# Kernel tuning notes

Hardware: AMD Instinct MI355X
Metric: run time of the kernel (lower is better)

Reference implementation:

```python
import jax, jax.numpy as jnp
import numpy as np

B, S, D, H = 2, 2048, 1024, 16
DK = D // H


def setup_inputs() -> dict:
    key = jax.random.key(0)
    ks = jax.random.split(key, 8)
    q = jax.random.normal(ks[0], (B, S, D), dtype=jnp.float32)
    k = jax.random.normal(ks[1], (B, S, D), dtype=jnp.float32)
    v = jax.random.normal(ks[2], (B, S, D), dtype=jnp.float32)
    mask = jax.random.randint(ks[3], (B, 1, S, S), 0, 2, dtype=jnp.int32)
    sc = 1.0 / np.sqrt(D)
    Wq = jax.random.normal(ks[4], (D, D), dtype=jnp.float32) * sc
    Wk = jax.random.normal(ks[5], (D, D), dtype=jnp.float32) * sc
    Wv = jax.random.normal(ks[6], (D, D), dtype=jnp.float32) * sc
    Wo = jax.random.normal(ks[7], (D, D), dtype=jnp.float32) * sc
    return {"q": q, "k": k, "v": v, "mask": mask, "Wq": Wq, "Wk": Wk, "Wv": Wv, "Wo": Wo}


def reference(q, k, v, mask, Wq, Wk, Wv, Wo):
    # Linear projections (torch Linear: x @ W.T; bias=False). Weights here stored
    # as [D, D] applied as x @ W (equivalent parameterization).
    query = q @ Wq  # [B,S,D]
    key = k @ Wk
    value = v @ Wv
    # split heads -> [B,H,S,DK]
    query = query.reshape(B, S, H, DK).transpose(0, 2, 1, 3)
    key = key.reshape(B, S, H, DK).transpose(0, 2, 1, 3)
    value = value.reshape(B, S, H, DK).transpose(0, 2, 1, 3)
    scores = jnp.einsum('bhqd,bhkd->bhqk', query, key) / jnp.sqrt(jnp.float32(DK))
    scores = jnp.where(mask == 0, jnp.float32(-1e9), scores)
    probs = jax.nn.softmax(scores, axis=-1)  # dropout p=0.0 -> identity
    x = jnp.einsum('bhqk,bhkd->bhqd', probs, value)
    x = x.transpose(0, 2, 1, 3).reshape(B, S, D)
    return x @ Wo
```

## Files before the change

### kernel.cpp

```cpp
#include <hip/hip_runtime.h>
#include <hip/hip_bf16.h>
#include <math.h>

#define B_ 2
#define S_ 2048
#define D_ 1024
#define H_ 16
#define DK_ 64
#define SW_ (S_ / 64)

typedef unsigned short u16;
typedef unsigned int u32;
typedef unsigned long long u64;
typedef __attribute__((ext_vector_type(8))) short short8;
typedef __attribute__((ext_vector_type(4))) float float4_;
typedef __attribute__((ext_vector_type(4))) unsigned int uint4_;

static __device__ inline u16 f_to_bf16(float f) {
    union { float f; u32 i; } x; x.f = f;
    u32 r = x.i + 0x7fff + ((x.i >> 16) & 1);
    return (u16)(r >> 16);
}

static __device__ __forceinline__ u32 cvtpk(float a, float b) {
    u32 r;
    asm("v_cvt_pk_bf16_f32 %0, %1, %2" : "=v"(r) : "v"(a), "v"(b));
    return r;
}

static __device__ __forceinline__ float fast_exp2(float x) {
#if __has_builtin(__builtin_amdgcn_exp2f)
    return __builtin_amdgcn_exp2f(x);
#else
    return exp2f(x);
#endif
}

static __device__ inline void gl_lds16(const u16* g, u16* l) {
    __builtin_amdgcn_global_load_lds((const __attribute__((address_space(1))) void*)g,
                                     (__attribute__((address_space(3))) void*)l, 16, 0, 0);
}

__global__ __launch_bounds__(256) void prep(const float* __restrict__ q,
                                            const float* __restrict__ k,
                                            const float* __restrict__ v,
                                            const int* __restrict__ mask,
                                            const float* __restrict__ W0,
                                            const float* __restrict__ W1,
                                            const float* __restrict__ W2,
                                            const float* __restrict__ W3,
                                            u16* __restrict__ qb, u16* __restrict__ kb,
                                            u16* __restrict__ vb,
                                            u16* __restrict__ T0, u16* __restrict__ T1,
                                            u16* __restrict__ T2, u16* __restrict__ T3,
                                            u64* __restrict__ mpk) {
    __shared__ float tile[32][33];
    int gx = blockIdx.x, tid = threadIdx.x;
    if (gx < 6144) {
        int z = gx >> 11;
        int bx = gx & 2047;
        const float* s = (z == 0) ? q : ((z == 1) ? k : v);
        u16* d = (z == 0) ? qb : ((z == 1) ? kb : vb);
        int i = (bx * 256 + tid) * 8;
        #pragma unroll
        for (int j = 0; j < 8; ++j) d[i + j] = f_to_bf16(s[i + j]);
    } else if (gx < 10240) {
        int g2 = gx - 6144;
        int z = g2 >> 10;
        int rem = g2 & 1023;
        const float* W = (z == 0) ? W0 : ((z == 1) ? W1 : ((z == 2) ? W2 : W3));
        u16* Wt = (z == 0) ? T0 : ((z == 1) ? T1 : ((z == 2) ? T2 : T3));
        int k0 = (rem >> 5) * 32, n0 = (rem & 31) * 32;
        int tx = tid & 31, ty = tid >> 5;
        #pragma unroll
        for (int i2 = 0; i2 < 4; ++i2) {
            int row = ty + i2 * 8;
            tile[row][tx] = W[(size_t)(k0 + row) * D_ + n0 + tx];
        }
        __syncthreads();
        #pragma unroll
        for (int i2 = 0; i2 < 4; ++i2) {
            int row = ty + i2 * 8;
            Wt[(size_t)(n0 + row) * D_ + k0 + tx] = f_to_bf16(tile[tx][row]);
        }
    } else {
        int g3 = gx - 10240;
        int wv = (g3 * 256 + tid) >> 6;
        int lane = tid & 63;
        #pragma unroll
        for (int i2 = 0; i2 < 8; ++i2) {
            int wd = wv * 8 + i2;
            u64 bits = __ballot(mask[(size_t)wd * 64 + lane] != 0);
            if (lane == 0) mpk[wd] = bits;
        }
    }
}

static __device__ __forceinline__ void gemm128_body(u16* lds,
                                                    const u16* __restrict__ A,
                                                    const u16* __restrict__ Bt,
                                                    int K, float4_ (&acc)[4][4]) {
    u16* ldsA = lds;
    u16* ldsB = lds + 4096;
    int tm = blockIdx.x, tn = blockIdx.y;
    int t = threadIdx.x, l = t & 63;
    int w = t >> 6, wr = w >> 1, wc = w & 1;
    int colL = l & 15, grp = l >> 4;
    int sw4 = (grp ^ ((colL >> 1) & 3)) << 3;
    int f0 = t, f1 = t + 256;
    int row0 = f0 >> 2, kc0 = (((f0 & 3) ^ ((f0 >> 3) & 3)) << 3);
    int row1 = f1 >> 2, kc1 = (((f1 & 3) ^ ((f1 >> 3) & 3)) << 3);
    const u16* gA0 = A  + (size_t)(tm * 128 + row0) * K + kc0;
    const u16* gA1 = A  + (size_t)(tm * 128 + row1) * K + kc1;
    const u16* gB0 = Bt + (size_t)(tn * 128 + row0) * K + kc0;
    const u16* gB1 = Bt + (size_t)(tn * 128 + row1) * K + kc1;

    #pragma unroll
    for (int mi = 0; mi < 4; ++mi)
        #pragma unroll
        for (int ni = 0; ni < 4; ++ni)
            acc[mi][ni] = (float4_){0.f, 0.f, 0.f, 0.f};

    for (int k0 = 0; k0 < K; k0 += 32) {
        __syncthreads();
        gl_lds16(gA0 + k0, ldsA + f0 * 8);
        gl_lds16(gA1 + k0, ldsA + f1 * 8);
        gl_lds16(gB0 + k0, ldsB + f0 * 8);
        gl_lds16(gB1 + k0, ldsB + f1 * 8);
        __syncthreads();
        short8 a[4], b[4];
        #pragma unroll
        for (int mi = 0; mi < 4; ++mi)
            a[mi] = *(const short8*)&ldsA[(wr * 64 + mi * 16 + colL) * 32 + sw4];
        #pragma unroll
        for (int ni = 0; ni < 4; ++ni)
            b[ni] = *(const short8*)&ldsB[(wc * 64 + ni * 16 + colL) * 32 + sw4];
        #pragma unroll
        for (int mi = 0; mi < 4; ++mi)
            #pragma unroll
            for (int ni = 0; ni < 4; ++ni)
                acc[mi][ni] = __builtin_amdgcn_mfma_f32_16x16x32_bf16(a[mi], b[ni], acc[mi][ni], 0, 0, 0);
    }
}

__global__ __launch_bounds__(256, 3) void gemm_qkv(const u16* __restrict__ qb,
                                                   const u16* __restrict__ kb,
                                                   const u16* __restrict__ vb,
                                                   const u16* __restrict__ Wqt,
                                                   const u16* __restrict__ Wkt,
                                                   const u16* __restrict__ Wvt,
                                                   u16* __restrict__ Qp,
                                                   u16* __restrict__ Kp,
                                                   u16* __restrict__ Vt) {
    __shared__ u16 lds[8192];
    int z = blockIdx.z;
    const u16* A  = (z == 0) ? qb  : ((z == 1) ? kb  : vb);
    const u16* Bt = (z == 0) ? Wqt : ((z == 1) ? Wkt : Wvt);
    float4_ acc[4][4];
    gemm128_body(lds, A, Bt, D_, acc);

    int tm = blockIdx.x, tn = blockIdx.y;
    int t = threadIdx.x, l = t & 63;
    int w = t >> 6, wr = w >> 1, wc = w & 1;
    int colL = l & 15, grp = l >> 4;

    if (z < 2) {
        u16* Y = (z == 0) ? Qp : Kp;
        float sc = (z == 0) ? (0.125f * 1.44269504f) : 1.0f;
        #pragma unroll
        for (int mi = 0; mi < 4; ++mi)
            #pragma unroll
            for (int ni = 0; ni < 4; ++ni)
                #pragma unroll
                for (int r = 0; r < 4; ++r)
                    Y[(size_t)(tm * 128 + wr * 64 + mi * 16 + grp * 4 + r) * D_
                      + tn * 128 + wc * 64 + ni * 16 + colL] = f_to_bf16(acc[mi][ni][r] * sc);
    } else {
        int tok_base = tm * 128 + wr * 64;
        int bb = tok_base >> 11;
        int s_hi = tok_base & (S_ - 1);
        #pragma unroll
        for (int mi = 0; mi < 4; ++mi)
            #pragma unroll
            for (int ni = 0; ni < 4; ++ni) {
                int n  = tn * 128 + wc * 64 + ni * 16 + colL;
                int hh = n >> 6, dk = n & 63;
                u16* vp = Vt + ((size_t)(bb * H_ + hh) * DK_ + dk) * S_ + s_hi;
                #pragma unroll
                for (int r = 0; r < 4; ++r) {
                    int m = mi * 16 + grp * 4 + r;
                    int mp_ = ((m >> 5) & 1) * 32 + ((m >> 2) & 3) * 8 + ((m >> 4) & 1) * 4 + (m & 3);
                    vp[mp_] = f_to_bf16(acc[mi][ni][r]);
                }
            }
    }
}

__global__ __launch_bounds__(256, 3) void gemm_out(const u16* __restrict__ Xa,
                                                   const u16* __restrict__ Wot,
                                                   float* __restrict__ out) {
    __shared__ u16 lds[8192];
    float4_ acc[4][4];
    gemm128_body(lds, Xa, Wot, D_, acc);

    int tm = blockIdx.x, tn = blockIdx.y;
    int t = threadIdx.x, l = t & 63;
    int w = t >> 6, wr = w >> 1, wc = w & 1;
    int colL = l & 15, grp = l >> 4;
    #pragma unroll
    for (int mi = 0; mi < 4; ++mi)
        #pragma unroll
        for (int ni = 0; ni < 4; ++ni)
            #pragma unroll
            for (int r = 0; r < 4; ++r)
                out[(size_t)(tm * 128 + wr * 64 + mi * 16 + grp * 4 + r) * D_
                    + tn * 128 + wc * 64 + ni * 16 + colL] = acc[mi][ni][r];
}

__global__ __launch_bounds__(256, 2) void attn128(const u16* __restrict__ Qp,
                                                  const u16* __restrict__ Kp,
                                                  const u16* __restrict__ Vt,
                                                  const u64* __restrict__ mp,
                                                  u16* __restrict__ Xa) {
    __shared__ u16 ldsK[2 * 128 * 64];
    __shared__ u16 ldsV[2 * 2 * 64 * 64];

    int bid = blockIdx.x;
    int qt = bid & 15, h = (bid >> 4) & 15, b = bid >> 8;
    int t = threadIdx.x, l = t & 63, w = t >> 6;
    int colL = l & 15, grp = l >> 4;

    const u16* qbA = Qp + (size_t)(b * S_ + qt * 128 + w * 32 + colL) * D_ + h * DK_;
    const u16* qbB = qbA + (size_t)16 * D_;
    short8 qfA0 = *(const short8*)(qbA + grp * 8);
    short8 qfA1 = *(const short8*)(qbA + 32 + grp * 8);
    short8 qfB0 = *(const short8*)(qbB + grp * 8);
    short8 qfB1 = *(const short8*)(qbB + 32 + grp * 8);

    const u16* gK[4];
    const u16* gV[4];
    int fofs[4];
    #pragma unroll
    for (int i = 0; i < 4; ++i) {
        int f = t + 256 * i;
        fofs[i] = f * 8;
        int krow = f >> 3, kch = (((f & 7) ^ (krow & 7)) << 3);
        gK[i] = Kp + (size_t)(b * S_ + krow) * D_ + h * DK_ + kch;
        int hreg = f >> 9, fp = f & 511;
        int vrow = fp >> 3, vch = (((fp & 7) ^ (vrow & 7)) << 3);
        gV[i] = Vt + ((size_t)(b * H_ + h) * DK_ + vrow) * S_ + hreg * 64 + vch;
    }

    int sw8 = (grp ^ (colL & 7)) << 3;

    short8 onesb;
    #pragma unroll
    for (int j = 0; j < 8; ++j) onesb[j] = (short)0x3F80;

    float4_ laccA = (float4_){0.f, 0.f, 0.f, 0.f};
    float4_ laccB = (float4_){0.f, 0.f, 0.f, 0.f};
    float4_ oA[4], oB[4];
    #pragma unroll
    for (int nt = 0; nt < 4; ++nt) {
        oA[nt] = (float4_){0.f, 0.f, 0.f, 0.f};
        oB[nt] = (float4_){0.f, 0.f, 0.f, 0.f};
    }

    const u64* mrA = mp + (size_t)(b * S_ + qt * 128 + w * 32 + colL) * SW_;
    const u64* mrB = mrA + (size_t)16 * SW_;

    #pragma unroll
    for (int i = 0; i < 4; ++i) {
        gl_lds16(gK[i], ldsK + fofs[i]);
        gl_lds16(gV[i], ldsV + fofs[i]);
    }
    __syncthreads();

    int cur = 0;
    for (int kt = 0; kt < S_; kt += 128) {
        u64 mwA0 = mrA[(kt >> 6)];
        u64 mwA1 = mrA[(kt >> 6) + 1];
        u64 mwB0 = mrB[(kt >> 6)];
        u64 mwB1 = mrB[(kt >> 6) + 1];

        if (kt + 128 < S_) {
            int nb = (cur ^ 1) * 8192;
            #pragma unroll
            for (int i = 0; i < 4; ++i) {
                gl_lds16(gK[i] + (size_t)(kt + 128) * D_, ldsK + nb + fofs[i]);
                gl_lds16(gV[i] + (kt + 128),              ldsV + nb + fofs[i]);
            }
        }

        const u16* K_ = ldsK + cur * 8192;
        const u16* V_ = ldsV + cur * 8192;

        float4_ sA[8], sB[8];
        __builtin_amdgcn_s_setprio(1);
        #pragma unroll
        for (int nt = 0; nt < 8; ++nt) {
            int ro = (nt * 16 + colL) * 64;
            short8 kf0 = *(const short8*)&K_[ro + sw8];
            short8 kf1 = *(const short8*)&K_[ro + (sw8 ^ 32)];
            sA[nt] = (float4_){0.f, 0.f, 0.f, 0.f};
            sA[nt] = __builtin_amdgcn_mfma_f32_16x16x32_bf16(kf0, qfA0, sA[nt], 0, 0, 0);
            sA[nt] = __builtin_amdgcn_mfma_f32_16x16x32_bf16(kf1, qfA1, sA[nt], 0, 0, 0);
            sB[nt] = (float4_){0.f, 0.f, 0.f, 0.f};
            sB[nt] = __builtin_amdgcn_mfma_f32_16x16x32_bf16(kf0, qfB0, sB[nt], 0, 0, 0);
            sB[nt] = __builtin_amdgcn_mfma_f32_16x16x32_bf16(kf1, qfB1, sB[nt], 0, 0, 0);
        }
        __builtin_amdgcn_s_setprio(0);

        u64 mshA0 = mwA0 >> (grp * 4), mshA1 = mwA1 >> (grp * 4);
        u64 mshB0 = mwB0 >> (grp * 4), mshB1 = mwB1 >> (grp * 4);
        #pragma unroll
        for (int nt = 0; nt < 8; ++nt) {
            u32 bitsA = ((u32)((nt < 4 ? mshA0 : mshA1) >> ((nt & 3) * 16))) & 15u;
            u32 bitsB = ((u32)((nt < 4 ? mshB0 : mshB1) >> ((nt & 3) * 16))) & 15u;
            #pragma unroll
            for (int r = 0; r < 4; ++r) {
                float pA = fast_exp2(sA[nt][r]);
                float pB = fast_exp2(sB[nt][r]);
                u32 keepA = 0u - ((bitsA >> r) & 1u);
                u32 keepB = 0u - ((bitsB >> r) & 1u);
                union { float f; u32 i; } ua, ub;
                ua.f = pA; ua.i &= keepA; sA[nt][r] = ua.f;
                ub.f = pB; ub.i &= keepB; sB[nt][r] = ub.f;
            }
        }

        short8 pfA[4], pfB[4];
        #pragma unroll
        for (int j = 0; j < 4; ++j) {
            uint4_ Ax = { cvtpk(sA[2 * j][0], sA[2 * j][1]), cvtpk(sA[2 * j][2], sA[2 * j][3]),
                          cvtpk(sA[2 * j + 1][0], sA[2 * j + 1][1]), cvtpk(sA[2 * j + 1][2], sA[2 * j + 1][3]) };
            pfA[j] = __builtin_bit_cast(short8, Ax);
            uint4_ Bx = { cvtpk(sB[2 * j][0], sB[2 * j][1]), cvtpk(sB[2 * j][2], sB[2 * j][3]),
                          cvtpk(sB[2 * j + 1][0], sB[2 * j + 1][1]), cvtpk(sB[2 * j + 1][2], sB[2 * j + 1][3]) };
            pfB[j] = __builtin_bit_cast(short8, Bx);
        }

        __builtin_amdgcn_s_setprio(1);
        #pragma unroll
        for (int nt = 0; nt < 4; ++nt) {
            int ro = (nt * 16 + colL) * 64;
            short8 vf0 = *(const short8*)&V_[ro + sw8];
            short8 vf1 = *(const short8*)&V_[ro + (sw8 ^ 32)];
            short8 vf2 = *(const short8*)&V_[4096 + ro + sw8];
            short8 vf3 = *(const short8*)&V_[4096 + ro + (sw8 ^ 32)];
            oA[nt] = __builtin_amdgcn_mfma_f32_16x16x32_bf16(pfA[0], vf0, oA[nt], 0, 0, 0);
            oA[nt] = __builtin_amdgcn_mfma_f32_16x16x32_bf16(pfA[1], vf1, oA[nt], 0, 0, 0);
            oA[nt] = __builtin_amdgcn_mfma_f32_16x16x32_bf16(pfA[2], vf2, oA[nt], 0, 0, 0);
            oA[nt] = __builtin_amdgcn_mfma_f32_16x16x32_bf16(pfA[3], vf3, oA[nt], 0, 0, 0);
            oB[nt] = __builtin_amdgcn_mfma_f32_16x16x32_bf16(pfB[0], vf0, oB[nt], 0, 0, 0);
            oB[nt] = __builtin_amdgcn_mfma_f32_16x16x32_bf16(pfB[1], vf1, oB[nt], 0, 0, 0);
            oB[nt] = __builtin_amdgcn_mfma_f32_16x16x32_bf16(pfB[2], vf2, oB[nt], 0, 0, 0);
            oB[nt] = __builtin_amdgcn_mfma_f32_16x16x32_bf16(pfB[3], vf3, oB[nt], 0, 0, 0);
        }
        laccA = __builtin_amdgcn_mfma_f32_16x16x32_bf16(pfA[0], onesb, laccA, 0, 0, 0);
        laccA = __builtin_amdgcn_mfma_f32_16x16x32_bf16(pfA[1], onesb, laccA, 0, 0, 0);
        laccA = __builtin_amdgcn_mfma_f32_16x16x32_bf16(pfA[2], onesb, laccA, 0, 0, 0);
        laccA = __builtin_amdgcn_mfma_f32_16x16x32_bf16(pfA[3], onesb, laccA, 0, 0, 0);
        laccB = __builtin_amdgcn_mfma_f32_16x16x32_bf16(pfB[0], onesb, laccB, 0, 0, 0);
        laccB = __builtin_amdgcn_mfma_f32_16x16x32_bf16(pfB[1], onesb, laccB, 0, 0, 0);
        laccB = __builtin_amdgcn_mfma_f32_16x16x32_bf16(pfB[2], onesb, laccB, 0, 0, 0);
        laccB = __builtin_amdgcn_mfma_f32_16x16x32_bf16(pfB[3], onesb, laccB, 0, 0, 0);
        __builtin_amdgcn_s_setprio(0);

        __syncthreads();
        cur ^= 1;
    }

    float invA[4], invB[4];
    #pragma unroll
    for (int r = 0; r < 4; ++r) {
        invA[r] = 1.f / laccA[r];
        invB[r] = 1.f / laccB[r];
    }

    u16* xoA = Xa + (size_t)(b * S_ + qt * 128 + w * 32 + grp * 4) * D_ + h * DK_;
    u16* xoB = xoA + (size_t)16 * D_;
    #pragma unroll
    for (int r = 0; r < 4; ++r)
        #pragma unroll
        for (int nt = 0; nt < 4; ++nt) {
            xoA[(size_t)r * D_ + nt * 16 + colL] = f_to_bf16(oA[nt][r] * invA[r]);
            xoB[(size_t)r * D_ + nt * 16 + colL] = f_to_bf16(oB[nt][r] * invB[r]);
        }
}

extern "C" void kernel_launch(void* const* d_in, const int* in_sizes, int n_in,
                              void* d_out, int out_size, void* d_ws, size_t ws_size,
                              hipStream_t stream) {
    const float* q    = (const float*)d_in[0];
    const float* k    = (const float*)d_in[1];
    const float* v    = (const float*)d_in[2];
    const int*   mask = (const int*)d_in[3];
    const float* Wq   = (const float*)d_in[4];
    const float* Wk   = (const float*)d_in[5];
    const float* Wv   = (const float*)d_in[6];
    const float* Wo   = (const float*)d_in[7];
    float* out = (float*)d_out;

    const int NQ = B_ * S_ * D_;
    const int NW = D_ * D_;

    u16* qb  = (u16*)d_ws;
    u16* kb  = qb  + NQ;
    u16* vb  = kb  + NQ;
    u16* Wqt = vb  + NQ;
    u16* Wkt = Wqt + NW;
    u16* Wvt = Wkt + NW;
    u16* Wot = Wvt + NW;
    u16* Qp  = Wot + NW;
    u16* Kp  = Qp  + NQ;
    u16* Vt  = Kp  + NQ;
    u16* Xa  = Vt  + NQ;
    u64* mpk = (u64*)(Xa + NQ);

    dim3 cblk(256);
    prep<<<14336, cblk, 0, stream>>>(q, k, v, mask, Wq, Wk, Wv, Wo,
                                     qb, kb, vb, Wqt, Wkt, Wvt, Wot, mpk);

    const int M = B_ * S_;
    gemm_qkv<<<dim3(M / 128, D_ / 128, 3), cblk, 0, stream>>>(qb, kb, vb, Wqt, Wkt, Wvt, Qp, Kp, Vt);

    attn128<<<B_ * H_ * (S_ / 128), cblk, 0, stream>>>(Qp, Kp, Vt, mpk, Xa);

    gemm_out<<<dim3(M / 128, D_ / 128), cblk, 0, stream>>>(Xa, Wot, out);
}
```

Measured before the change: 244.9 us.

## Double-buffer GEMM LDS tiles and use fine-grained vmcnt waits in attention

The shared GEMM body now keeps two LDS buffers, prefetching the next K-slice while MFMAs consume the current one. Its two __syncthreads per step become an s_waitcnt vmcnt plus raw s_barrier, so global-to-LDS latency can overlap compute. The attention kernel gets the same treatment: explicit vmcnt counts let the current tile's loads complete while the next prefetch stays in flight, and its block index is remapped to change the order heads and batches are scheduled across CUs. The cost is doubled GEMM LDS usage, which may limit occupancy, and correctness now depends on hand-counted outstanding loads.

```diff
diff --git a/kernel.cpp b/kernel.cpp
--- a/kernel.cpp
+++ b/kernel.cpp
@@ -101,7 +101,7 @@
                                                     const u16* __restrict__ Bt,
                                                     int K, float4_ (&acc)[4][4]) {
     u16* ldsA = lds;
-    u16* ldsB = lds + 4096;
+    u16* ldsB = lds + 8192;
     int tm = blockIdx.x, tn = blockIdx.y;
     int t = threadIdx.x, l = t & 63;
     int w = t >> 6, wr = w >> 1, wc = w & 1;
@@ -121,25 +121,39 @@
         for (int ni = 0; ni < 4; ++ni)
             acc[mi][ni] = (float4_){0.f, 0.f, 0.f, 0.f};
 
+    gl_lds16(gA0, ldsA + f0 * 8);
+    gl_lds16(gA1, ldsA + f1 * 8);
+    gl_lds16(gB0, ldsB + f0 * 8);
+    gl_lds16(gB1, ldsB + f1 * 8);
+
     for (int k0 = 0; k0 < K; k0 += 32) {
-        __syncthreads();
-        gl_lds16(gA0 + k0, ldsA + f0 * 8);
-        gl_lds16(gA1 + k0, ldsA + f1 * 8);
-        gl_lds16(gB0 + k0, ldsB + f0 * 8);
-        gl_lds16(gB1 + k0, ldsB + f1 * 8);
-        __syncthreads();
+        int cur = (k0 >> 5) & 1;
+        if (k0 + 32 < K) {
+            int nb = (cur ^ 1) * 4096;
+            gl_lds16(gA0 + k0 + 32, ldsA + nb + f0 * 8);
+            gl_lds16(gA1 + k0 + 32, ldsA + nb + f1 * 8);
+            gl_lds16(gB0 + k0 + 32, ldsB + nb + f0 * 8);
+            gl_lds16(gB1 + k0 + 32, ldsB + nb + f1 * 8);
+            asm volatile("s_waitcnt vmcnt(4)" ::: "memory");
+        } else {
+            asm volatile("s_waitcnt vmcnt(0)" ::: "memory");
+        }
+        __builtin_amdgcn_s_barrier();
+        const u16* cA = ldsA + cur * 4096;
+        const u16* cB = ldsB + cur * 4096;
         short8 a[4], b[4];
         #pragma unroll
         for (int mi = 0; mi < 4; ++mi)
-            a[mi] = *(const short8*)&ldsA[(wr * 64 + mi * 16 + colL) * 32 + sw4];
+            a[mi] = *(const short8*)&cA[(wr * 64 + mi * 16 + colL) * 32 + sw4];
         #pragma unroll
         for (int ni = 0; ni < 4; ++ni)
-            b[ni] = *(const short8*)&ldsB[(wc * 64 + ni * 16 + colL) * 32 + sw4];
+            b[ni] = *(const short8*)&cB[(wc * 64 + ni * 16 + colL) * 32 + sw4];
         #pragma unroll
         for (int mi = 0; mi < 4; ++mi)
             #pragma unroll
             for (int ni = 0; ni < 4; ++ni)
                 acc[mi][ni] = __builtin_amdgcn_mfma_f32_16x16x32_bf16(a[mi], b[ni], acc[mi][ni], 0, 0, 0);
+        __builtin_amdgcn_s_barrier();
     }
 }
 
@@ -152,7 +166,7 @@
                                                    u16* __restrict__ Qp,
                                                    u16* __restrict__ Kp,
                                                    u16* __restrict__ Vt) {
-    __shared__ u16 lds[8192];
+    __shared__ u16 lds[16384];
     int z = blockIdx.z;
     const u16* A  = (z == 0) ? qb  : ((z == 1) ? kb  : vb);
     const u16* Bt = (z == 0) ? Wqt : ((z == 1) ? Wkt : Wvt);
@@ -199,7 +213,7 @@
 __global__ __launch_bounds__(256, 3) void gemm_out(const u16* __restrict__ Xa,
                                                    const u16* __restrict__ Wot,
                                                    float* __restrict__ out) {
-    __shared__ u16 lds[8192];
+    __shared__ u16 lds[16384];
     float4_ acc[4][4];
     gemm128_body(lds, Xa, Wot, D_, acc);
 
@@ -225,7 +239,8 @@
     __shared__ u16 ldsK[2 * 128 * 64];
     __shared__ u16 ldsV[2 * 2 * 64 * 64];
 
-    int bid = blockIdx.x;
+    int bid0 = blockIdx.x;
+    int bid = ((bid0 & 7) << 6) | (bid0 >> 3);
     int qt = bid & 15, h = (bid >> 4) & 15, b = bid >> 8;
     int t = threadIdx.x, l = t & 63, w = t >> 6;
     int colL = l & 15, grp = l >> 4;
@@ -274,10 +289,10 @@
         gl_lds16(gK[i], ldsK + fofs[i]);
         gl_lds16(gV[i], ldsV + fofs[i]);
     }
-    __syncthreads();
-
-    int cur = 0;
+
     for (int kt = 0; kt < S_; kt += 128) {
+        int cur = (kt >> 7) & 1;
+
         u64 mwA0 = mrA[(kt >> 6)];
         u64 mwA1 = mrA[(kt >> 6) + 1];
         u64 mwB0 = mrB[(kt >> 6)];
@@ -290,7 +305,11 @@
                 gl_lds16(gK[i] + (size_t)(kt + 128) * D_, ldsK + nb + fofs[i]);
                 gl_lds16(gV[i] + (kt + 128),              ldsV + nb + fofs[i]);
             }
-        }
+            asm volatile("s_waitcnt vmcnt(12)" ::: "memory");
+        } else {
+            asm volatile("s_waitcnt vmcnt(4)" ::: "memory");
+        }
+        __builtin_amdgcn_s_barrier();
 
         const u16* K_ = ldsK + cur * 8192;
         const u16* V_ = ldsV + cur * 8192;
@@ -367,8 +386,7 @@
         laccB = __builtin_amdgcn_mfma_f32_16x16x32_bf16(pfB[3], onesb, laccB, 0, 0, 0);
         __builtin_amdgcn_s_setprio(0);
 
-        __syncthreads();
-        cur ^= 1;
+        __builtin_amdgcn_s_barrier();
     }
 
     float invA[4], invB[4];
```

Result: faster. 238.5 us (-2.6%).
